# Kernel optimization log

Measured on AMD Instinct MI355X. Metric: run time of the kernel, lower is better.

Reference implementation:

```python
import jax, jax.numpy as jnp
import numpy as np

B, H, S, D = 4, 16, 2048, 64
TEMPERATURE = 8.0  # sqrt(D)
NEG = -1000000000.0

def setup_inputs() -> dict:
    key = jax.random.key(0)
    kq, kk, kv, km = jax.random.split(key, 4)
    q = jax.random.normal(kq, (B, H, S, D), dtype=jnp.float32)
    k = jax.random.normal(kk, (B, H, S, D), dtype=jnp.float32)
    v = jax.random.normal(kv, (B, H, S, D), dtype=jnp.float32)
    mask = jax.random.randint(km, (B, 1, S, S), 0, 2, dtype=jnp.int32)
    return {"q": q, "k": k, "v": v, "mask": mask}

def reference(q, k, v, mask):
    # scores: [B,H,S,S]
    scores = jnp.einsum('bhqd,bhkd->bhqk', q / TEMPERATURE, k)
    scores = jnp.where(mask == 1, NEG, scores)
    attn = jax.nn.softmax(scores, axis=-1)  # dropout p=0.0 -> identity
    out = jnp.einsum('bhqk,bhkd->bhqd', attn, v)
    return out
```

## Files before the change

### kernel.cpp

```cpp
#include <hip/hip_runtime.h>

#define NB 4
#define NH 16
#define SS 2048
#define DD 64
#define QT 256
#define KT 64
#define NT (SS / KT)
#define KSP 72
#define QSCALE 0.18033688011112042f

#define WS_BITS_BYTES ((size_t)NB * SS * (SS / 8))
#define WS_KB_OFF  ((size_t)2  << 20)
#define WS_VB_OFF  ((size_t)18 << 20)
#define WS_FULL    ((size_t)34 << 20)

typedef __bf16 bf16x8 __attribute__((ext_vector_type(8)));
typedef __bf16 bf16x2 __attribute__((ext_vector_type(2)));
typedef float  floatx16 __attribute__((ext_vector_type(16)));
typedef unsigned long long u64t;

static_assert(sizeof(bf16x8) == 16, "bf16x8 must be 16B");

__device__ __forceinline__ int pack2(float a, float b) {
    bf16x2 v; v[0] = (__bf16)a; v[1] = (__bf16)b;
    return __builtin_bit_cast(int, v);
}

__device__ __forceinline__ int vperm_col(int k) {
    return 16 * (k >> 4) + 8 * ((k >> 2) & 1) + (k & 3) + 4 * ((k >> 3) & 1);
}
__device__ __forceinline__ int vperm_inv(int c) {
    return 16 * ((c >> 4) & 3) + 8 * ((c >> 2) & 1) + 4 * ((c >> 3) & 1) + (c & 3);
}

__global__ __launch_bounds__(256)
void pack_mask_kernel(const int* __restrict__ M, u64t* __restrict__ bits)
{
    const int w    = (blockIdx.x * 256 + threadIdx.x) >> 6;
    const int lane = threadIdx.x & 63;
    #pragma unroll 4
    for (int i = 0; i < 16; ++i) {
        const int gw   = i * 16384 + w;
        const size_t row = (size_t)(gw >> 5);
        const int word = gw & 31;
        const int mval = M[row * SS + (size_t)word * 64 + lane];
        const u64t b = __ballot(mval == 1);
        if (lane == 0) bits[gw] = b;
    }
}

__global__ __launch_bounds__(256)
void pre_kernel(const float* __restrict__ K, const float* __restrict__ V,
                const int* __restrict__ M, u64t* __restrict__ bits,
                __bf16* __restrict__ KB, __bf16* __restrict__ VB)
{
    __shared__ float vt[64][68];
    const int t = threadIdx.x;

    if (blockIdx.x < 2048) {
        const int bh = blockIdx.x >> 5;
        const int tt = blockIdx.x & 31;
        const size_t tb = (size_t)bh * SS * DD + (size_t)tt * (KT * DD);

        {
            const float* src = K + tb + t * 16;
            __bf16* dst = KB + tb + t * 16;
            float4 f0 = ((const float4*)src)[0];
            float4 f1 = ((const float4*)src)[1];
            float4 f2 = ((const float4*)src)[2];
            float4 f3 = ((const float4*)src)[3];
            bf16x8 o0, o1;
            o0[0]=(__bf16)f0.x; o0[1]=(__bf16)f0.y; o0[2]=(__bf16)f0.z; o0[3]=(__bf16)f0.w;
            o0[4]=(__bf16)f1.x; o0[5]=(__bf16)f1.y; o0[6]=(__bf16)f1.z; o0[7]=(__bf16)f1.w;
            o1[0]=(__bf16)f2.x; o1[1]=(__bf16)f2.y; o1[2]=(__bf16)f2.z; o1[3]=(__bf16)f2.w;
            o1[4]=(__bf16)f3.x; o1[5]=(__bf16)f3.y; o1[6]=(__bf16)f3.z; o1[7]=(__bf16)f3.w;
            ((bf16x8*)dst)[0] = o0;
            ((bf16x8*)dst)[1] = o1;
        }

        {
            const int key = t >> 2, ds = (t & 3) * 16;
            const float* src = V + tb + (size_t)key * DD + ds;
            #pragma unroll
            for (int i = 0; i < 4; ++i)
                *(float4*)&vt[key][ds + 4 * i] = ((const float4*)src)[i];
        }
        __syncthreads();
        {
            const int dim = t >> 2, cb = (t & 3) * 16;
            bf16x8 o0, o1;
            #pragma unroll
            for (int c = 0; c < 16; ++c) {
                const float vvv = vt[vperm_inv(cb + c)][dim];
                if (c < 8) o0[c] = (__bf16)vvv; else o1[c - 8] = (__bf16)vvv;
            }
            __bf16* dst = VB + tb + (size_t)dim * 64 + cb;
            ((bf16x8*)dst)[0] = o0;
            ((bf16x8*)dst)[1] = o1;
        }
    } else {
        const int w    = ((blockIdx.x - 2048) * 256 + t) >> 6;
        const int lane = t & 63;
        #pragma unroll 4
        for (int i = 0; i < 16; ++i) {
            const int gw   = i * 16384 + w;
            const size_t row = (size_t)(gw >> 5);
            const int word = gw & 31;
            const int mval = M[row * SS + (size_t)word * 64 + lane];
            const u64t b = __ballot(mval == 1);
            if (lane == 0) bits[gw] = b;
        }
    }
}

__global__ __launch_bounds__(256, 2)
void attn2_kernel(const float* __restrict__ Q, const unsigned* __restrict__ MBu,
                  const __bf16* __restrict__ KB, const __bf16* __restrict__ VB,
                  float* __restrict__ O)
{
    __shared__ __bf16 ks [2][KT][KSP];
    __shared__ __bf16 vsT[2][DD][KSP];

    const int t    = threadIdx.x;
    const int wave = t >> 6;
    const int lane = t & 63;
    const int l31  = lane & 31;
    const int h8   = lane >> 5;

    const int bh    = blockIdx.x & 63;
    const int qtile = blockIdx.x >> 6;
    const int b     = bh >> 4;
    const int q0    = qtile * QT + wave * 64;

    const size_t base = (size_t)bh * SS * DD;

    bf16x8 aqA[4], aqB[4];
    #pragma unroll
    for (int grp = 0; grp < 2; ++grp) {
        const float* qp = Q + base + (size_t)(q0 + 32 * grp + l31) * DD + 8 * h8;
        #pragma unroll
        for (int s = 0; s < 4; ++s) {
            float4 f0 = *(const float4*)(qp + 16 * s);
            float4 f1 = *(const float4*)(qp + 16 * s + 4);
            bf16x8 a;
            a[0] = (__bf16)(f0.x * QSCALE); a[1] = (__bf16)(f0.y * QSCALE);
            a[2] = (__bf16)(f0.z * QSCALE); a[3] = (__bf16)(f0.w * QSCALE);
            a[4] = (__bf16)(f1.x * QSCALE); a[5] = (__bf16)(f1.y * QSCALE);
            a[6] = (__bf16)(f1.z * QSCALE); a[7] = (__bf16)(f1.w * QSCALE);
            if (grp == 0) aqA[s] = a; else aqB[s] = a;
        }
    }

    bf16x8 ones8;
    #pragma unroll
    for (int i = 0; i < 8; ++i) ones8[i] = (__bf16)1.0f;

    const int srow = t >> 3;
    const int sc8  = (t & 7) * 8;
    const __bf16* kbp = KB + base + (size_t)srow * DD + sc8;
    const __bf16* vbp = VB + base + (size_t)srow * DD + sc8;
    bf16x8 kr0, kr1, vr0, vr1;

    kr0 = *(const bf16x8*)kbp;
    kr1 = *(const bf16x8*)(kbp + 32 * DD);
    vr0 = *(const bf16x8*)vbp;
    vr1 = *(const bf16x8*)(vbp + 32 * DD);

    const u64t* mbrA = (const u64t*)MBu + ((size_t)b * SS + q0 + l31)      * (SS / 64);
    const u64t* mbrB = (const u64t*)MBu + ((size_t)b * SS + q0 + 32 + l31) * (SS / 64);
    u64t mA = mbrA[0], mB = mbrB[0], mnA, mnB;

    floatx16 o0A, o1A, oLA, o0B, o1B, oLB;
    #pragma unroll
    for (int i = 0; i < 16; ++i) {
        o0A[i] = 0.f; o1A[i] = 0.f; oLA[i] = 0.f;
        o0B[i] = 0.f; o1B[i] = 0.f; oLB[i] = 0.f;
    }

    for (int tt = 0; tt < NT; ++tt) {
        const int cur = tt & 1;

        *(bf16x8*)&ks [cur][srow]     [sc8] = kr0;
        *(bf16x8*)&ks [cur][srow + 32][sc8] = kr1;
        *(bf16x8*)&vsT[cur][srow]     [sc8] = vr0;
        *(bf16x8*)&vsT[cur][srow + 32][sc8] = vr1;

        asm volatile("s_waitcnt lgkmcnt(0)" ::: "memory");
        __builtin_amdgcn_s_barrier();
        asm volatile("" ::: "memory");

        {
            const size_t jn = (size_t)((tt + 1) & (NT - 1)) * (KT * DD);
            kr0 = *(const bf16x8*)(kbp + jn);
            kr1 = *(const bf16x8*)(kbp + jn + 32 * DD);
            vr0 = *(const bf16x8*)(vbp + jn);
            vr1 = *(const bf16x8*)(vbp + jn + 32 * DD);
        }
        mnA = mbrA[(tt + 1) & (NT - 1)];
        mnB = mbrB[(tt + 1) & (NT - 1)];

        #pragma unroll
        for (int half = 0; half < 2; ++half) {
            floatx16 cA, cB;
            {
                const unsigned uA = (unsigned)(mA >> (32 * half)) >> (4 * h8);
                const unsigned uB = (unsigned)(mB >> (32 * half)) >> (4 * h8);
                #pragma unroll
                for (int i = 0; i < 16; ++i) {
                    const int pos = (i & 3) + 8 * (i >> 2);
                    const int sA = ((int)(uA << (31 - pos))) >> 31;
                    const int sB = ((int)(uB << (31 - pos))) >> 31;
                    cA[i] = __builtin_bit_cast(float, sA & (int)0xC4800000u);
                    cB[i] = __builtin_bit_cast(float, sB & (int)0xC4800000u);
                }
            }

            __builtin_amdgcn_s_setprio(1);
            #pragma unroll
            for (int s = 0; s < 4; ++s) {
                bf16x8 a = *(const bf16x8*)&ks[cur][32 * half + l31][16 * s + 8 * h8];
                cA = __builtin_amdgcn_mfma_f32_32x32x16_bf16(a, aqA[s], cA, 0, 0, 0);
                cB = __builtin_amdgcn_mfma_f32_32x32x16_bf16(a, aqB[s], cB, 0, 0, 0);
            }
            __builtin_amdgcn_s_setprio(0);

            int pkA[8], pkB[8];
            #pragma unroll
            for (int g = 0; g < 8; ++g) {
                float a0 = __builtin_amdgcn_exp2f(cA[2 * g]);
                float a1 = __builtin_amdgcn_exp2f(cA[2 * g + 1]);
                float b0 = __builtin_amdgcn_exp2f(cB[2 * g]);
                float b1 = __builtin_amdgcn_exp2f(cB[2 * g + 1]);
                pkA[g] = pack2(a0, a1);
                pkB[g] = pack2(b0, b1);
            }

            __builtin_amdgcn_s_setprio(1);
            #pragma unroll
            for (int s2 = 0; s2 < 2; ++s2) {
                bf16x8 av0 = *(const bf16x8*)&vsT[cur][l31]     [32 * half + 16 * s2 + 8 * h8];
                bf16x8 av1 = *(const bf16x8*)&vsT[cur][32 + l31][32 * half + 16 * s2 + 8 * h8];
                int4 fwA; fwA.x = pkA[4*s2]; fwA.y = pkA[4*s2+1]; fwA.z = pkA[4*s2+2]; fwA.w = pkA[4*s2+3];
                int4 fwB; fwB.x = pkB[4*s2]; fwB.y = pkB[4*s2+1]; fwB.z = pkB[4*s2+2]; fwB.w = pkB[4*s2+3];
                bf16x8 bpA = __builtin_bit_cast(bf16x8, fwA);
                bf16x8 bpB = __builtin_bit_cast(bf16x8, fwB);
                o0A = __builtin_amdgcn_mfma_f32_32x32x16_bf16(av0, bpA, o0A, 0, 0, 0);
                o0B = __builtin_amdgcn_mfma_f32_32x32x16_bf16(av0, bpB, o0B, 0, 0, 0);
                o1A = __builtin_amdgcn_mfma_f32_32x32x16_bf16(av1, bpA, o1A, 0, 0, 0);
                o1B = __builtin_amdgcn_mfma_f32_32x32x16_bf16(av1, bpB, o1B, 0, 0, 0);
                oLA = __builtin_amdgcn_mfma_f32_32x32x16_bf16(ones8, bpA, oLA, 0, 0, 0);
                oLB = __builtin_amdgcn_mfma_f32_32x32x16_bf16(ones8, bpB, oLB, 0, 0, 0);
            }
            __builtin_amdgcn_s_setprio(0);
        }

        mA = mnA; mB = mnB;
    }

    const float invA = 1.0f / oLA[0];
    const float invB = 1.0f / oLB[0];
    float* opA = O + base + (size_t)(q0 + l31) * DD;
    float* opB = O + base + (size_t)(q0 + 32 + l31) * DD;
    #pragma unroll
    for (int s = 0; s < 4; ++s) {
        float4 st;
        st.x = o0A[4*s+0] * invA; st.y = o0A[4*s+1] * invA;
        st.z = o0A[4*s+2] * invA; st.w = o0A[4*s+3] * invA;
        *(float4*)(opA + 8 * s + 4 * h8) = st;
        st.x = o1A[4*s+0] * invA; st.y = o1A[4*s+1] * invA;
        st.z = o1A[4*s+2] * invA; st.w = o1A[4*s+3] * invA;
        *(float4*)(opA + 32 + 8 * s + 4 * h8) = st;
        st.x = o0B[4*s+0] * invB; st.y = o0B[4*s+1] * invB;
        st.z = o0B[4*s+2] * invB; st.w = o0B[4*s+3] * invB;
        *(float4*)(opB + 8 * s + 4 * h8) = st;
        st.x = o1B[4*s+0] * invB; st.y = o1B[4*s+1] * invB;
        st.z = o1B[4*s+2] * invB; st.w = o1B[4*s+3] * invB;
        *(float4*)(opB + 32 + 8 * s + 4 * h8) = st;
    }
}

template<int MODE>
__global__ __launch_bounds__(512, 4)
void attn_kernel(const float* __restrict__ Q, const float* __restrict__ K,
                 const float* __restrict__ V, const int* __restrict__ M,
                 const unsigned* __restrict__ MB, float* __restrict__ O)
{
    __shared__ __bf16 ks [2][KT][KSP];
    __shared__ __bf16 vsT[2][DD][KSP];

    const int t    = threadIdx.x;
    const int wave = t >> 6;
    const int lane = t & 63;
    const int l31  = lane & 31;
    const int h8   = lane >> 5;

    const int bh    = blockIdx.x & 63;
    const int qtile = blockIdx.x >> 6;
    const int b     = bh >> 4;
    const int q0    = qtile * QT + wave * 32;

    const size_t base = (size_t)bh * SS * DD;

    bf16x8 aq[4];
    {
        const float* qp = Q + base + (size_t)(q0 + l31) * DD + 8 * h8;
        #pragma unroll
        for (int s = 0; s < 4; ++s) {
            float4 f0 = *(const float4*)(qp + 16 * s);
            float4 f1 = *(const float4*)(qp + 16 * s + 4);
            bf16x8 a;
            a[0] = (__bf16)(f0.x * QSCALE); a[1] = (__bf16)(f0.y * QSCALE);
            a[2] = (__bf16)(f0.z * QSCALE); a[3] = (__bf16)(f0.w * QSCALE);
            a[4] = (__bf16)(f1.x * QSCALE); a[5] = (__bf16)(f1.y * QSCALE);
            a[6] = (__bf16)(f1.z * QSCALE); a[7] = (__bf16)(f1.w * QSCALE);
            aq[s] = a;
        }
    }

    bf16x8 ones8;
    #pragma unroll
    for (int i = 0; i < 8; ++i) ones8[i] = (__bf16)1.0f;

    const int skey = t >> 3;
    const int sdc  = (t & 7) * 8;
    const int vk   = 2 * (t & 31);
    const int vdc  = (t >> 5) * 4;
    const int vcol = vperm_col(vk);
    const float* kp0 = K + base + (size_t)skey * DD + sdc;
    const float* vp0 = V + base + (size_t)vk * DD + vdc;

    float4 ka0 = ((const float4*)kp0)[0];
    float4 ka1 = ((const float4*)kp0)[1];
    float4 va0 = *(const float4*)(vp0);
    float4 va1 = *(const float4*)(vp0 + DD);

    const u64t* mbrow = (const u64t*)MB + ((size_t)b * SS + q0 + l31) * (SS / 64);
    const int*  mrow  = M + (size_t)b * SS * SS + (size_t)(q0 + l31) * SS + 4 * h8;
    u64t mall = 0, mnext = 0;
    if constexpr (MODE >= 1) mall = mbrow[0];

    floatx16 o0, o1, oL;
    #pragma unroll
    for (int i = 0; i < 16; ++i) { o0[i] = 0.f; o1[i] = 0.f; oL[i] = 0.f; }

    for (int tt = 0; tt < NT; ++tt) {
        const int cur = tt & 1;

        {
            bf16x8 kw;
            kw[0]=(__bf16)ka0.x; kw[1]=(__bf16)ka0.y; kw[2]=(__bf16)ka0.z; kw[3]=(__bf16)ka0.w;
            kw[4]=(__bf16)ka1.x; kw[5]=(__bf16)ka1.y; kw[6]=(__bf16)ka1.z; kw[7]=(__bf16)ka1.w;
            *(bf16x8*)&ks[cur][skey][sdc] = kw;
            #pragma unroll
            for (int i = 0; i < 4; ++i) {
                bf16x2 pr;
                pr[0] = (__bf16)(&va0.x)[i]; pr[1] = (__bf16)(&va1.x)[i];
                *(bf16x2*)&vsT[cur][vdc + i][vcol] = pr;
            }
        }
        __syncthreads();

        int4 mi[8];
        if constexpr (MODE == 0) {
            #pragma unroll
            for (int g = 0; g < 8; ++g)
                mi[g] = *(const int4*)(mrow + tt * KT + 8 * g);
        }

        {
            const int jn = ((tt + 1) * KT) & (SS - 1);
            const float* kn = kp0 + (size_t)jn * DD;
            ka0 = ((const float4*)kn)[0];
            ka1 = ((const float4*)kn)[1];
            const float* vn = vp0 + (size_t)jn * DD;
            va0 = *(const float4*)(vn);
            va1 = *(const float4*)(vn + DD);
        }
        if constexpr (MODE >= 1) mnext = mbrow[(tt + 1) & (NT - 1)];

        #pragma unroll
        for (int half = 0; half < 2; ++half) {
            floatx16 c;
            if constexpr (MODE >= 1) {
                const unsigned u = (unsigned)(mall >> (32 * half)) >> (4 * h8);
                #pragma unroll
                for (int i = 0; i < 16; ++i) {
                    const int pos = (i & 3) + 8 * (i >> 2);
                    const int sm = ((int)(u << (31 - pos))) >> 31;
                    c[i] = __builtin_bit_cast(float, sm & (int)0xC4800000u);
                }
            } else {
                #pragma unroll
                for (int i = 0; i < 16; ++i) {
                    const int g2 = 4 * half + (i >> 2);
                    c[i] = ((&mi[g2].x)[i & 3] == 1) ? -1024.0f : 0.0f;
                }
            }

            __builtin_amdgcn_s_setprio(1);
            #pragma unroll
            for (int s = 0; s < 4; ++s) {
                bf16x8 a = *(const bf16x8*)&ks[cur][32 * half + l31][16 * s + 8 * h8];
                c = __builtin_amdgcn_mfma_f32_32x32x16_bf16(a, aq[s], c, 0, 0, 0);
            }
            __builtin_amdgcn_s_setprio(0);

            int pk[8];
            #pragma unroll
            for (int g = 0; g < 8; ++g) {
                float pa = __builtin_amdgcn_exp2f(c[2 * g]);
                float pb = __builtin_amdgcn_exp2f(c[2 * g + 1]);
                pk[g] = pack2(pa, pb);
            }

            __builtin_amdgcn_s_setprio(1);
            #pragma unroll
            for (int s2 = 0; s2 < 2; ++s2) {
                int4 fw; fw.x = pk[4*s2]; fw.y = pk[4*s2+1]; fw.z = pk[4*s2+2]; fw.w = pk[4*s2+3];
                bf16x8 bp = __builtin_bit_cast(bf16x8, fw);
                bf16x8 av0 = *(const bf16x8*)&vsT[cur][l31]     [32 * half + 16 * s2 + 8 * h8];
                bf16x8 av1 = *(const bf16x8*)&vsT[cur][32 + l31][32 * half + 16 * s2 + 8 * h8];
                o0 = __builtin_amdgcn_mfma_f32_32x32x16_bf16(av0, bp, o0, 0, 0, 0);
                o1 = __builtin_amdgcn_mfma_f32_32x32x16_bf16(av1, bp, o1, 0, 0, 0);
                oL = __builtin_amdgcn_mfma_f32_32x32x16_bf16(ones8, bp, oL, 0, 0, 0);
            }
            __builtin_amdgcn_s_setprio(0);
        }

        if constexpr (MODE >= 1) mall = mnext;
    }

    float inv = 1.0f / oL[0];
    float* op = O + base + (size_t)(q0 + l31) * DD;
    #pragma unroll
    for (int s = 0; s < 4; ++s) {
        float4 st0, st1;
        st0.x = o0[4*s+0] * inv; st0.y = o0[4*s+1] * inv;
        st0.z = o0[4*s+2] * inv; st0.w = o0[4*s+3] * inv;
        st1.x = o1[4*s+0] * inv; st1.y = o1[4*s+1] * inv;
        st1.z = o1[4*s+2] * inv; st1.w = o1[4*s+3] * inv;
        *(float4*)(op + 8 * s + 4 * h8)      = st0;
        *(float4*)(op + 32 + 8 * s + 4 * h8) = st1;
    }
}

extern "C" void kernel_launch(void* const* d_in, const int* in_sizes, int n_in,
                              void* d_out, int out_size, void* d_ws, size_t ws_size,
                              hipStream_t stream) {
    (void)in_sizes; (void)n_in; (void)out_size;
    const float* q = (const float*)d_in[0];
    const float* k = (const float*)d_in[1];
    const float* v = (const float*)d_in[2];
    const int*   m = (const int*)d_in[3];
    float* out = (float*)d_out;
    dim3 grid(NB * NH * (SS / QT));

    if (ws_size >= WS_FULL) {
        u64t*   bits = (u64t*)d_ws;
        __bf16* kb16 = (__bf16*)((char*)d_ws + WS_KB_OFF);
        __bf16* vb16 = (__bf16*)((char*)d_ws + WS_VB_OFF);
        pre_kernel<<<dim3(6144), 256, 0, stream>>>(k, v, m, bits, kb16, vb16);
        attn2_kernel<<<grid, 256, 0, stream>>>(q, (const unsigned*)bits,
                                               kb16, vb16, out);
    } else if (ws_size >= WS_BITS_BYTES) {
        u64t* bits = (u64t*)d_ws;
        pack_mask_kernel<<<dim3(4096), 256, 0, stream>>>(m, bits);
        attn_kernel<1><<<grid, 512, 0, stream>>>(q, k, v, m, (const unsigned*)bits, out);
    } else {
        attn_kernel<0><<<grid, 512, 0, stream>>>(q, k, v, m, nullptr, out);
    }
}
```

Baseline: 271.4 us.

## Replace ones-MFMA row sum with VALU accumulation and restructure QK schedule

Removes the extra MFMA that multiplied the probability tile by a ones matrix to get softmax denominators. Instead each lane accumulates the fp32 exp values in registers and combines the two half-waves with a shuffle at the end. The loop is also restructured so that all K fragments are loaded and both QK halves computed up front, followed by two exp+PV phases. This cuts matrix-core work by about a fifth, at the cost of more live registers (four score accumulators at once) and extra VALU adds. The denominator is now summed from unrounded fp32 values rather than bf16-rounded ones, which changes numerics slightly.

After: 270.1 us. About the same (-0.5%).

```diff
diff --git a/kernel.cpp b/kernel.cpp
--- a/kernel.cpp
+++ b/kernel.cpp
@@ -123,10 +123,10 @@
     __shared__ __bf16 vsT[2][DD][KSP];
 
     const int t    = threadIdx.x;
-    const int wave = t >> 6;
     const int lane = t & 63;
     const int l31  = lane & 31;
     const int h8   = lane >> 5;
+    const int wave = t >> 6;
 
     const int bh    = blockIdx.x & 63;
     const int qtile = blockIdx.x >> 6;
@@ -152,10 +152,6 @@
         }
     }
 
-    bf16x8 ones8;
-    #pragma unroll
-    for (int i = 0; i < 8; ++i) ones8[i] = (__bf16)1.0f;
-
     const int srow = t >> 3;
     const int sc8  = (t & 7) * 8;
     const __bf16* kbp = KB + base + (size_t)srow * DD + sc8;
@@ -171,12 +167,12 @@
     const u64t* mbrB = (const u64t*)MBu + ((size_t)b * SS + q0 + 32 + l31) * (SS / 64);
     u64t mA = mbrA[0], mB = mbrB[0], mnA, mnB;
 
-    floatx16 o0A, o1A, oLA, o0B, o1B, oLB;
+    floatx16 o0A, o1A, o0B, o1B;
     #pragma unroll
     for (int i = 0; i < 16; ++i) {
-        o0A[i] = 0.f; o1A[i] = 0.f; oLA[i] = 0.f;
-        o0B[i] = 0.f; o1B[i] = 0.f; oLB[i] = 0.f;
-    }
+        o0A[i] = 0.f; o1A[i] = 0.f; o0B[i] = 0.f; o1B[i] = 0.f;
+    }
+    float lsA = 0.f, lsB = 0.f;
 
     for (int tt = 0; tt < NT; ++tt) {
         const int cur = tt & 1;
@@ -200,66 +196,108 @@
         mnA = mbrA[(tt + 1) & (NT - 1)];
         mnB = mbrB[(tt + 1) & (NT - 1)];
 
-        #pragma unroll
-        for (int half = 0; half < 2; ++half) {
-            floatx16 cA, cB;
-            {
-                const unsigned uA = (unsigned)(mA >> (32 * half)) >> (4 * h8);
-                const unsigned uB = (unsigned)(mB >> (32 * half)) >> (4 * h8);
-                #pragma unroll
-                for (int i = 0; i < 16; ++i) {
-                    const int pos = (i & 3) + 8 * (i >> 2);
-                    const int sA = ((int)(uA << (31 - pos))) >> 31;
-                    const int sB = ((int)(uB << (31 - pos))) >> 31;
-                    cA[i] = __builtin_bit_cast(float, sA & (int)0xC4800000u);
-                    cB[i] = __builtin_bit_cast(float, sB & (int)0xC4800000u);
-                }
-            }
-
-            __builtin_amdgcn_s_setprio(1);
-            #pragma unroll
-            for (int s = 0; s < 4; ++s) {
-                bf16x8 a = *(const bf16x8*)&ks[cur][32 * half + l31][16 * s + 8 * h8];
-                cA = __builtin_amdgcn_mfma_f32_32x32x16_bf16(a, aqA[s], cA, 0, 0, 0);
-                cB = __builtin_amdgcn_mfma_f32_32x32x16_bf16(a, aqB[s], cB, 0, 0, 0);
-            }
-            __builtin_amdgcn_s_setprio(0);
-
-            int pkA[8], pkB[8];
+        __builtin_amdgcn_s_setprio(1);
+
+        bf16x8 kf0[4], kf1[4];
+        #pragma unroll
+        for (int s = 0; s < 4; ++s) {
+            kf0[s] = *(const bf16x8*)&ks[cur][l31]     [16 * s + 8 * h8];
+            kf1[s] = *(const bf16x8*)&ks[cur][32 + l31][16 * s + 8 * h8];
+        }
+
+        floatx16 cA0, cB0, cA1, cB1;
+        {
+            const unsigned uA0 = (unsigned)(mA)       >> (4 * h8);
+            const unsigned uB0 = (unsigned)(mB)       >> (4 * h8);
+            const unsigned uA1 = (unsigned)(mA >> 32) >> (4 * h8);
+            const unsigned uB1 = (unsigned)(mB >> 32) >> (4 * h8);
+            #pragma unroll
+            for (int i = 0; i < 16; ++i) {
+                const int pos = (i & 3) + 8 * (i >> 2);
+                cA0[i] = __builtin_bit_cast(float, (((int)(uA0 << (31 - pos))) >> 31) & (int)0xC4800000u);
+                cB0[i] = __builtin_bit_cast(float, (((int)(uB0 << (31 - pos))) >> 31) & (int)0xC4800000u);
+                cA1[i] = __builtin_bit_cast(float, (((int)(uA1 << (31 - pos))) >> 31) & (int)0xC4800000u);
+                cB1[i] = __builtin_bit_cast(float, (((int)(uB1 << (31 - pos))) >> 31) & (int)0xC4800000u);
+            }
+        }
+
+        #pragma unroll
+        for (int s = 0; s < 4; ++s) {
+            cA0 = __builtin_amdgcn_mfma_f32_32x32x16_bf16(kf0[s], aqA[s], cA0, 0, 0, 0);
+            cB0 = __builtin_amdgcn_mfma_f32_32x32x16_bf16(kf0[s], aqB[s], cB0, 0, 0, 0);
+            cA1 = __builtin_amdgcn_mfma_f32_32x32x16_bf16(kf1[s], aqA[s], cA1, 0, 0, 0);
+            cB1 = __builtin_amdgcn_mfma_f32_32x32x16_bf16(kf1[s], aqB[s], cB1, 0, 0, 0);
+        }
+
+        int pkA0[8], pkB0[8];
+        {
+            float sa0 = 0.f, sa1 = 0.f, sb0 = 0.f, sb1 = 0.f;
             #pragma unroll
             for (int g = 0; g < 8; ++g) {
-                float a0 = __builtin_amdgcn_exp2f(cA[2 * g]);
-                float a1 = __builtin_amdgcn_exp2f(cA[2 * g + 1]);
-                float b0 = __builtin_amdgcn_exp2f(cB[2 * g]);
-                float b1 = __builtin_amdgcn_exp2f(cB[2 * g + 1]);
-                pkA[g] = pack2(a0, a1);
-                pkB[g] = pack2(b0, b1);
-            }
-
-            __builtin_amdgcn_s_setprio(1);
-            #pragma unroll
-            for (int s2 = 0; s2 < 2; ++s2) {
-                bf16x8 av0 = *(const bf16x8*)&vsT[cur][l31]     [32 * half + 16 * s2 + 8 * h8];
-                bf16x8 av1 = *(const bf16x8*)&vsT[cur][32 + l31][32 * half + 16 * s2 + 8 * h8];
-                int4 fwA; fwA.x = pkA[4*s2]; fwA.y = pkA[4*s2+1]; fwA.z = pkA[4*s2+2]; fwA.w = pkA[4*s2+3];
-                int4 fwB; fwB.x = pkB[4*s2]; fwB.y = pkB[4*s2+1]; fwB.z = pkB[4*s2+2]; fwB.w = pkB[4*s2+3];
-                bf16x8 bpA = __builtin_bit_cast(bf16x8, fwA);
-                bf16x8 bpB = __builtin_bit_cast(bf16x8, fwB);
-                o0A = __builtin_amdgcn_mfma_f32_32x32x16_bf16(av0, bpA, o0A, 0, 0, 0);
-                o0B = __builtin_amdgcn_mfma_f32_32x32x16_bf16(av0, bpB, o0B, 0, 0, 0);
-                o1A = __builtin_amdgcn_mfma_f32_32x32x16_bf16(av1, bpA, o1A, 0, 0, 0);
-                o1B = __builtin_amdgcn_mfma_f32_32x32x16_bf16(av1, bpB, o1B, 0, 0, 0);
-                oLA = __builtin_amdgcn_mfma_f32_32x32x16_bf16(ones8, bpA, oLA, 0, 0, 0);
-                oLB = __builtin_amdgcn_mfma_f32_32x32x16_bf16(ones8, bpB, oLB, 0, 0, 0);
-            }
-            __builtin_amdgcn_s_setprio(0);
-        }
+                float a0 = __builtin_amdgcn_exp2f(cA0[2 * g]);
+                float a1 = __builtin_amdgcn_exp2f(cA0[2 * g + 1]);
+                float b0 = __builtin_amdgcn_exp2f(cB0[2 * g]);
+                float b1 = __builtin_amdgcn_exp2f(cB0[2 * g + 1]);
+                sa0 += a0; sa1 += a1; sb0 += b0; sb1 += b1;
+                pkA0[g] = pack2(a0, a1);
+                pkB0[g] = pack2(b0, b1);
+            }
+            lsA += sa0 + sa1; lsB += sb0 + sb1;
+        }
+
+        #pragma unroll
+        for (int s2 = 0; s2 < 2; ++s2) {
+            bf16x8 av0 = *(const bf16x8*)&vsT[cur][l31]     [16 * s2 + 8 * h8];
+            bf16x8 av1 = *(const bf16x8*)&vsT[cur][32 + l31][16 * s2 + 8 * h8];
+            int4 fwA; fwA.x = pkA0[4*s2]; fwA.y = pkA0[4*s2+1]; fwA.z = pkA0[4*s2+2]; fwA.w = pkA0[4*s2+3];
+            int4 fwB; fwB.x = pkB0[4*s2]; fwB.y = pkB0[4*s2+1]; fwB.z = pkB0[4*s2+2]; fwB.w = pkB0[4*s2+3];
+            bf16x8 bpA = __builtin_bit_cast(bf16x8, fwA);
+            bf16x8 bpB = __builtin_bit_cast(bf16x8, fwB);
+            o0A = __builtin_amdgcn_mfma_f32_32x32x16_bf16(av0, bpA, o0A, 0, 0, 0);
+            o0B = __builtin_amdgcn_mfma_f32_32x32x16_bf16(av0, bpB, o0B, 0, 0, 0);
+            o1A = __builtin_amdgcn_mfma_f32_32x32x16_bf16(av1, bpA, o1A, 0, 0, 0);
+            o1B = __builtin_amdgcn_mfma_f32_32x32x16_bf16(av1, bpB, o1B, 0, 0, 0);
+        }
+
+        int pkA1[8], pkB1[8];
+        {
+            float sa0 = 0.f, sa1 = 0.f, sb0 = 0.f, sb1 = 0.f;
+            #pragma unroll
+            for (int g = 0; g < 8; ++g) {
+                float a0 = __builtin_amdgcn_exp2f(cA1[2 * g]);
+                float a1 = __builtin_amdgcn_exp2f(cA1[2 * g + 1]);
+                float b0 = __builtin_amdgcn_exp2f(cB1[2 * g]);
+                float b1 = __builtin_amdgcn_exp2f(cB1[2 * g + 1]);
+                sa0 += a0; sa1 += a1; sb0 += b0; sb1 += b1;
+                pkA1[g] = pack2(a0, a1);
+                pkB1[g] = pack2(b0, b1);
+            }
+            lsA += sa0 + sa1; lsB += sb0 + sb1;
+        }
+
+        #pragma unroll
+        for (int s2 = 0; s2 < 2; ++s2) {
+            bf16x8 av0 = *(const bf16x8*)&vsT[cur][l31]     [32 + 16 * s2 + 8 * h8];
+            bf16x8 av1 = *(const bf16x8*)&vsT[cur][32 + l31][32 + 16 * s2 + 8 * h8];
+            int4 fwA; fwA.x = pkA1[4*s2]; fwA.y = pkA1[4*s2+1]; fwA.z = pkA1[4*s2+2]; fwA.w = pkA1[4*s2+3];
+            int4 fwB; fwB.x = pkB1[4*s2]; fwB.y = pkB1[4*s2+1]; fwB.z = pkB1[4*s2+2]; fwB.w = pkB1[4*s2+3];
+            bf16x8 bpA = __builtin_bit_cast(bf16x8, fwA);
+            bf16x8 bpB = __builtin_bit_cast(bf16x8, fwB);
+            o0A = __builtin_amdgcn_mfma_f32_32x32x16_bf16(av0, bpA, o0A, 0, 0, 0);
+            o0B = __builtin_amdgcn_mfma_f32_32x32x16_bf16(av0, bpB, o0B, 0, 0, 0);
+            o1A = __builtin_amdgcn_mfma_f32_32x32x16_bf16(av1, bpA, o1A, 0, 0, 0);
+            o1B = __builtin_amdgcn_mfma_f32_32x32x16_bf16(av1, bpB, o1B, 0, 0, 0);
+        }
+
+        __builtin_amdgcn_s_setprio(0);
 
         mA = mnA; mB = mnB;
     }
 
-    const float invA = 1.0f / oLA[0];
-    const float invB = 1.0f / oLB[0];
+    lsA += __shfl_xor(lsA, 32);
+    lsB += __shfl_xor(lsB, 32);
+    const float invA = 1.0f / lsA;
+    const float invB = 1.0f / lsB;
     float* opA = O + base + (size_t)(q0 + l31) * DD;
     float* opB = O + base + (size_t)(q0 + 32 + l31) * DD;
     #pragma unroll
```
